# Kernel optimization log

Hardware: AMD Instinct MI355X
Metric: run time of the kernel (lower is better)

Reference implementation:

```python
import jax, jax.numpy as jnp
import numpy as np

N_BATCH, CH, HW, KERNEL, STRIDE, VC = 8, 256, 96, 8, 3, 512


def setup_inputs() -> dict:
    key = jax.random.key(0)
    k0, k1, k2, k3 = jax.random.split(key, 4)
    kk = KERNEL * KERNEL
    x = jax.random.normal(k0, (N_BATCH, CH, HW, HW), dtype=jnp.float32)
    # 1x1 conv weight [vc, ch, 1, 1] stored as [vc, ch]
    conv_w = jax.random.normal(k1, (VC, CH), dtype=jnp.float32) * 0.05
    # integrate_mask_activation: Linear(ch+kk, 3ch) -> LeakyReLU(0.2) -> Linear(3ch, ch) -> Tanh
    W1 = jax.random.normal(k2, (3 * CH, CH + kk), dtype=jnp.float32) * 0.02
    b1 = jnp.zeros((3 * CH,), dtype=jnp.float32)
    W2 = jax.random.normal(k3, (CH, 3 * CH), dtype=jnp.float32) * 0.02
    b2 = jnp.zeros((CH,), dtype=jnp.float32)
    return {"x": x, "conv_w": conv_w, "W1": W1, "b1": b1, "W2": W2, "b2": b2}


def _unfold(x, k, s):
    # torch.nn.Unfold(kernel=(k,k), stride=s) -> patches [n, L, c, k, k]
    n, c, h, w = x.shape
    oh = (h - k) // s + 1
    ow = (w - k) // s + 1
    ih = (jnp.arange(oh) * s)[:, None] + jnp.arange(k)[None, :]  # [oh, k]
    iw = (jnp.arange(ow) * s)[:, None] + jnp.arange(k)[None, :]  # [ow, k]
    p = x[:, :, ih, :]          # [n, c, oh, k, w]
    p = p[:, :, :, :, iw]       # [n, c, oh, k, ow, k]
    p = p.transpose(0, 2, 4, 1, 3, 5)  # [n, oh, ow, c, k, k]
    return p.reshape(n, oh * ow, c, k, k), oh * ow


def reference(x, conv_w, W1, b1, W2, b2):
    k = KERNEL
    kk = k * k
    n, c, h, w = x.shape
    patches, L = _unfold(x, k, STRIDE)           # [n, L, c, k, k]
    N = n * L
    p = patches.reshape(N, c, k, k)

    # GenerateMask_2_0: normalized similarity via 1x1 conv
    x_norm = jnp.sqrt((p ** 2).sum(1))           # [N, k, k]
    w_norm = jnp.sqrt((conv_w ** 2).sum(1))      # [vc]
    y = jnp.einsum('nchw,vc->nvhw', p, conv_w)   # [N, vc, k, k]
    y = y / (x_norm[:, None, :, :] * w_norm[None, :, None, None])

    vc = conv_w.shape[0]
    y_flat = y.reshape(N, vc * kk)
    idx = jnp.argmax(y_flat, axis=1)                       # topk(k=1)
    max_sim = jnp.take_along_axis(y_flat, idx[:, None], axis=1)  # [N, 1]
    max_ch = idx // kk                                     # codebook index [N]
    col = idx % kk                                         # spatial index [N]

    rows = jnp.arange(N)
    sim_map_max = y.reshape(N, vc, kk)[rows, max_ch]       # [N, kk]
    max_act = p.reshape(N, c, kk)[rows, :, col]            # [N, c]
    vc_vec = conv_w[max_ch]                                # [N, c]
    integ = max_act * max_sim + vc_vec * (1.0 - max_sim)   # blend with codebook

    # integrate_mask_activation MLP
    inp = jnp.concatenate([integ, sim_map_max], axis=1)    # [N, c + kk]
    h1 = inp @ W1.T + b1
    h1 = jnp.where(h1 > 0, h1, 0.2 * h1)                   # LeakyReLU(0.2)
    out = jnp.tanh(h1 @ W2.T + b2)                         # [N, c]
    return out.reshape(n, L, c)
```

## Files before the change

### kernel.cpp

```cpp
#include <hip/hip_runtime.h>
#include <hip/hip_fp16.h>
#include <math.h>

#define NB 8
#define CHN 256
#define HWD 96
#define PIXN (HWD*HWD)
#define TOTPIX (NB*PIXN)
#define VCN 512
#define OHW 30
#define LPP (OHW*OHW)
#define NPATCH (NB*LPP)
#define INPD 320
#define HID 768
#define MTP 456

typedef unsigned short u16;
typedef __attribute__((ext_vector_type(8))) short bf16x8;
typedef __attribute__((ext_vector_type(8))) unsigned short us8;
typedef __attribute__((ext_vector_type(4))) float f32x4;

__device__ __forceinline__ float f4c(const float4 v, int i){
  return i==0 ? v.x : i==1 ? v.y : i==2 ? v.z : v.w;
}
__device__ __forceinline__ u16 bfrn(float f){
  unsigned u = __float_as_uint(f);
  return (u16)((u + 0x7fffu + ((u>>16)&1u)) >> 16);
}
__device__ __forceinline__ float bf2f(u16 h){
  return __uint_as_float(((unsigned)h)<<16);
}


template<int NS>
__global__ __launch_bounds__(64) void wsplit_k(const float* __restrict__ src,
                                               u16* __restrict__ dst, int K){
  const int rt = blockIdx.x, kk = blockIdx.y, kkc = gridDim.y;
  const int lane = threadIdx.x, qr = lane>>4, col = lane&15;
  const float* s = src + (size_t)(rt*16+col)*K + kk*32 + qr*8;
  us8 h1, h2, h3;
  #pragma unroll
  for (int j=0;j<8;j++){
    float a = s[j];
    u16 x1 = bfrn(a);  float r1 = a - bf2f(x1);
    u16 x2 = bfrn(r1); float r2 = r1 - bf2f(x2);
    h1[j]=x1; h2[j]=x2; h3[j]=bfrn(r2);
  }
  size_t base = ((size_t)(rt*kkc + kk)*NS)*512 + lane*8;
  *(us8*)&dst[base]     = h1;
  *(us8*)&dst[base+512] = h2;
  if (NS == 3) *(us8*)&dst[base+1024] = h3;
}

__global__ void wnorm_k(const float* __restrict__ cw, float* __restrict__ invw){
  int v = blockIdx.x*256 + threadIdx.x;
  if (v >= VCN) return;
  const float* r = cw + (size_t)v*CHN;
  float s = 0.f;
  #pragma unroll 4
  for (int c=0;c<CHN;c++){ float t=r[c]; s = fmaf(t,t,s); }
  invw[v] = 1.0f/sqrtf(s);
}

__global__ void pixfin_k(const float* __restrict__ sumsq, float* __restrict__ invpix){
  int p = blockIdx.x*256 + threadIdx.x;
  if (p < TOTPIX) invpix[p] = rsqrtf(sumsq[p]);
}

__global__ __launch_bounds__(256) void xsplit_k(const float* __restrict__ x,
                                                u16* __restrict__ xf,
                                                float* __restrict__ sumsq){
  __shared__ float ts[64][65];
  __shared__ float ssq[64];
  const int p0 = blockIdx.x*64, c0 = blockIdx.y*64, img = blockIdx.z;
  const int t = threadIdx.x, lp = t&63, sub = t>>6;
  if (t < 64) ssq[t] = 0.f;
  const float* xb = x + (size_t)img*CHN*PIXN;
  #pragma unroll
  for (int r=0;r<16;r++){
    int cl = r*4 + sub;
    ts[cl][lp] = xb[(size_t)(c0+cl)*PIXN + p0 + lp];
  }
  __syncthreads();
  {
    float s = 0.f;
    #pragma unroll
    for (int r=0;r<16;r++){ float v = ts[r*4+sub][lp]; s = fmaf(v,v,s); }
    atomicAdd(&ssq[lp], s);
  }
  const int w = t>>6, lane = t&63;
  const int qr = lane>>4, pcol = lane&15;
  const size_t ptg = (size_t)(img*PIXN + p0)/16 + w;
  #pragma unroll
  for (int kkl=0;kkl<2;kkl++){
    const int kkg = (c0>>5) + kkl;
    us8 h1,h2,h3;
    #pragma unroll
    for (int j=0;j<8;j++){
      float a = ts[kkl*32 + qr*8 + j][w*16 + pcol];
      u16 x1 = bfrn(a);  float r1 = a - bf2f(x1);
      u16 x2 = bfrn(r1); float r2 = r1 - bf2f(x2);
      h1[j]=x1; h2[j]=x2; h3[j]=bfrn(r2);
    }
    size_t base = ((ptg*8 + kkg)*3)*512 + lane*8;
    *(us8*)&xf[base]      = h1;
    *(us8*)&xf[base+512]  = h2;
    *(us8*)&xf[base+1024] = h3;
  }
  __syncthreads();
  if (t < 64) atomicAdd(&sumsq[(size_t)img*PIXN + p0 + t], ssq[t]);
}

__global__ __launch_bounds__(256,4) void gemm_z_k(
    const u16* __restrict__ xf, const u16* __restrict__ wf,
    const float* __restrict__ invpix, const float* __restrict__ invw,
    float* __restrict__ mcand, int* __restrict__ vcand,
    __half* __restrict__ zf){
  __shared__ float rv[128][2];
  __shared__ int   ri[128][2];
  const int t = threadIdx.x;
  const int v0 = blockIdx.x*128, m0 = blockIdx.y*128;
  const int lane = t&63, wv = t>>6;
  const int mq = wv&1, nq = wv>>1;
  const int col = lane&15, qr = lane>>4;
  const size_t loff = (size_t)lane*8;
  const int ptA0 = (m0>>4) + mq*4;
  const int vtB0 = (v0>>4) + nq*4;
  f32x4 acc[4][4];
  #pragma unroll
  for (int i=0;i<4;i++)
    #pragma unroll
    for (int j=0;j<4;j++) acc[i][j] = (f32x4){0.f,0.f,0.f,0.f};

  for (int kk=0; kk<8; kk++){
    bf16x8 a[4][3];
    #pragma unroll
    for (int mi=0;mi<4;mi++){
      const size_t ab = (((size_t)(ptA0+mi)*8 + kk)*3)*512 + loff;
      a[mi][0] = *(const bf16x8*)&xf[ab];
      a[mi][1] = *(const bf16x8*)&xf[ab+512];
      a[mi][2] = *(const bf16x8*)&xf[ab+1024];
    }
    #pragma unroll
    for (int ni=0;ni<4;ni++){
      const size_t bb = (((size_t)(vtB0+ni)*8 + kk)*3)*512 + loff;
      const bf16x8 b1 = *(const bf16x8*)&wf[bb];
      const bf16x8 b2 = *(const bf16x8*)&wf[bb+512];
      const bf16x8 b3 = *(const bf16x8*)&wf[bb+1024];
      #pragma unroll
      for (int mi=0;mi<4;mi++){
        f32x4 c = acc[mi][ni];
        c = __builtin_amdgcn_mfma_f32_16x16x32_bf16(a[mi][0], b1, c, 0,0,0);
        c = __builtin_amdgcn_mfma_f32_16x16x32_bf16(a[mi][0], b2, c, 0,0,0);
        c = __builtin_amdgcn_mfma_f32_16x16x32_bf16(a[mi][1], b1, c, 0,0,0);
        c = __builtin_amdgcn_mfma_f32_16x16x32_bf16(a[mi][0], b3, c, 0,0,0);
        c = __builtin_amdgcn_mfma_f32_16x16x32_bf16(a[mi][1], b2, c, 0,0,0);
        c = __builtin_amdgcn_mfma_f32_16x16x32_bf16(a[mi][2], b1, c, 0,0,0);
        acc[mi][ni] = c;
      }
    }
  }
  float iw[4];
  #pragma unroll
  for (int ni=0; ni<4; ni++) iw[ni] = invw[v0 + nq*64 + ni*16 + col];
  #pragma unroll
  for (int mi=0; mi<4; mi++){
    #pragma unroll
    for (int r=0; r<4; r++){
      const int P = mq*64 + mi*16 + qr*4 + r;
      const float ip = invpix[m0 + P];
      float bz = -1e30f; int bvi = 0;
      #pragma unroll
      for (int ni=0; ni<4; ni++){
        const float z = f4c(*(const float4*)&acc[mi][ni], r) * ip * iw[ni];
        const int vv = v0 + nq*64 + ni*16 + col;
        zf[(size_t)(m0+P)*VCN + vv] = __float2half(z);
        if (z > bz){ bz = z; bvi = vv; }
      }
      #pragma unroll
      for (int off=1; off<16; off<<=1){
        const float oz = __shfl_xor(bz, off);
        const int  oi = __shfl_xor(bvi, off);
        if (oz > bz || (oz == bz && oi < bvi)){ bz = oz; bvi = oi; }
      }
      if (col == 0){ rv[P][nq] = bz; ri[P][nq] = bvi; }
    }
  }
  __syncthreads();
  if (t < 128){
    float z0 = rv[t][0], z1 = rv[t][1];
    int   i0 = ri[t][0], i1 = ri[t][1];
    float best = z0; int bi = i0;
    if (z1 > best || (z1 == best && i1 < bi)){ best = z1; bi = i1; }
    mcand[(size_t)(m0+t)*4 + blockIdx.x] = best;
    vcand[(size_t)(m0+t)*4 + blockIdx.x] = bi;
  }
}

__global__ __launch_bounds__(64) void select_k(
    const u16* __restrict__ xf, const float* __restrict__ cw,
    const __half* __restrict__ zf,
    const float* __restrict__ mcand, const int* __restrict__ vcand,
    u16* __restrict__ inpf){
  __shared__ float wlds[256];
  __shared__ float simv[64];
  const int q = blockIdx.x;
  const int lane = threadIdx.x;
  const int n = q / LPP, l = q % LPP;
  const int oy = l / OHW, ox = l % OHW;
  const int pl = (oy*3 + (lane >> 3))*HWD + (ox*3 + (lane & 7));
  const int p = n*PIXN + pl;
  const int rt = q >> 4, ql = q & 15;
  float best = -1e30f; int bv = 0;
  #pragma unroll
  for (int s=0;s<4;s++){
    float v2 = mcand[(size_t)p*4 + s];
    int i2 = vcand[(size_t)p*4 + s];
    if (v2 > best || (v2 == best && i2 < bv)){ best = v2; bv = i2; }
  }
  float val = best;
  int flat = bv*64 + lane;
  #pragma unroll
  for (int off=32; off>0; off>>=1){
    float ov = __shfl_xor(val, off);
    int of = __shfl_xor(flat, off);
    if (ov > val || (ov == val && of < flat)){ val = ov; flat = of; }
  }
  const int mch = flat >> 6;
  const int pos = flat & 63;
  const float ms = val;
  *(float4*)&wlds[lane*4] = *(const float4*)&cw[(size_t)mch*CHN + lane*4];
  simv[lane] = __half2float(zf[(size_t)p*VCN + mch]);
  __syncthreads();
  if (lane < 32){
    const int kk = lane >> 2, qr = lane & 3;
    const int wp = n*PIXN + (oy*3 + (pos>>3))*HWD + (ox*3 + (pos&7));
    const int wpt = wp >> 4, wpc = wp & 15;
    const size_t bb = (((size_t)wpt*8 + kk)*3)*512 + (qr*16 + wpc)*8;
    const us8 x1 = *(const us8*)&xf[bb];
    const us8 x2 = *(const us8*)&xf[bb+512];
    const us8 x3 = *(const us8*)&xf[bb+1024];
    const float om = 1.0f - ms;
    const int c0 = kk*32 + qr*8;
    us8 p1, p2;
    #pragma unroll
    for (int j=0;j<8;j++){
      float tv = bf2f(x1[j])+bf2f(x2[j])+bf2f(x3[j]);
      float v = fmaf(tv, ms, wlds[c0+j]*om);
      u16 s1 = bfrn(v);
      p1[j] = s1; p2[j] = bfrn(v - bf2f(s1));
    }
    const size_t ob = ((size_t)(rt*10 + kk)*2)*512 + (qr*16 + ql)*8;
    *(us8*)&inpf[ob]     = p1;
    *(us8*)&inpf[ob+512] = p2;
  }
  if (lane < 16){
    const int s = lane >> 3, kk = 8 + ((lane >> 2) & 1), qr = lane & 3;
    us8 pv;
    #pragma unroll
    for (int j=0;j<8;j++){
      float v = simv[(kk-8)*32 + qr*8 + j];
      u16 s1 = bfrn(v);
      pv[j] = (s == 0) ? s1 : bfrn(v - bf2f(s1));
    }
    const size_t ob = ((size_t)(rt*10 + kk)*2 + s)*512 + (qr*16 + ql)*8;
    *(us8*)&inpf[ob] = pv;
  }
}

__global__ __launch_bounds__(256,2) void mlp1_k(
    const u16* __restrict__ af, const u16* __restrict__ bf,
    const float* __restrict__ bias, u16* __restrict__ h1f){
  const int kkc = INPD >> 5;
  const int t = threadIdx.x;
  const int n0 = blockIdx.x*128, m0 = blockIdx.y*128;
  const int lane = t&63, wv = t>>6;
  const int mq = wv&1, nq = wv>>1;
  const int col = lane&15, qr = lane>>4;
  const size_t loff = (size_t)lane*8;
  const int ptA0 = (m0>>4) + mq*4;
  const int ntB0 = (n0>>4) + nq*4;
  f32x4 acc[4][4];
  #pragma unroll
  for (int i=0;i<4;i++)
    #pragma unroll
    for (int j=0;j<4;j++) acc[i][j] = (f32x4){0.f,0.f,0.f,0.f};

  for (int kk=0; kk<kkc; kk++){
    bf16x8 a[4][2];
    #pragma unroll
    for (int mi=0;mi<4;mi++){
      const size_t ab = (((size_t)(ptA0+mi)*kkc + kk)*2)*512 + loff;
      a[mi][0] = *(const bf16x8*)&af[ab];
      a[mi][1] = *(const bf16x8*)&af[ab+512];
    }
    #pragma unroll
    for (int ni=0;ni<4;ni++){
      const size_t bb = (((size_t)(ntB0+ni)*kkc + kk)*2)*512 + loff;
      const bf16x8 b1 = *(const bf16x8*)&bf[bb];
      const bf16x8 b2 = *(const bf16x8*)&bf[bb+512];
      #pragma unroll
      for (int mi=0;mi<4;mi++){
        f32x4 c = acc[mi][ni];
        c = __builtin_amdgcn_mfma_f32_16x16x32_bf16(a[mi][0], b1, c, 0,0,0);
        c = __builtin_amdgcn_mfma_f32_16x16x32_bf16(a[mi][0], b2, c, 0,0,0);
        c = __builtin_amdgcn_mfma_f32_16x16x32_bf16(a[mi][1], b1, c, 0,0,0);
        acc[mi][ni] = c;
      }
    }
  }
  float bb4[4];
  #pragma unroll
  for (int ni=0;ni<4;ni++) bb4[ni] = bias[n0 + nq*64 + ni*16 + col];
  #pragma unroll
  for (int mi=0;mi<4;mi++){
    const int rt2 = (m0>>4) + mq*4 + mi;
    #pragma unroll
    for (int r=0;r<4;r++){
      #pragma unroll
      for (int ni=0;ni<4;ni++){
        float v = f4c(*(const float4*)&acc[mi][ni], r) + bb4[ni];
        v = v > 0.f ? v : 0.2f*v;
        u16 s1 = bfrn(v);
        u16 s2 = bfrn(v - bf2f(s1));
        const int kk2 = (n0>>5) + nq*2 + (ni>>1);
        const int qn = (ni&1)*2 + (col>>3);
        const size_t ob = ((size_t)(rt2*24 + kk2)*2)*512 + (qn*16 + qr*4 + r)*8 + (col&7);
        h1f[ob] = s1; h1f[ob+512] = s2;
      }
    }
  }
}

__global__ __launch_bounds__(256,2) void mlp2_k(
    const u16* __restrict__ af, const u16* __restrict__ bf,
    const float* __restrict__ bias, float* __restrict__ C){
  const int kkc = HID >> 5;
  const int t = threadIdx.x;
  const int n0 = blockIdx.x*128, m0 = blockIdx.y*128;
  const int lane = t&63, wv = t>>6;
  const int mq = wv&1, nq = wv>>1;
  const int col = lane&15, qr = lane>>4;
  const size_t loff = (size_t)lane*8;
  const int ptA0 = (m0>>4) + mq*4;
  const int ntB0 = (n0>>4) + nq*4;
  f32x4 acc[4][4];
  #pragma unroll
  for (int i=0;i<4;i++)
    #pragma unroll
    for (int j=0;j<4;j++) acc[i][j] = (f32x4){0.f,0.f,0.f,0.f};

  for (int kk=0; kk<kkc; kk++){
    bf16x8 a[4][2];
    #pragma unroll
    for (int mi=0;mi<4;mi++){
      const size_t ab = (((size_t)(ptA0+mi)*kkc + kk)*2)*512 + loff;
      a[mi][0] = *(const bf16x8*)&af[ab];
      a[mi][1] = *(const bf16x8*)&af[ab+512];
    }
    #pragma unroll
    for (int ni=0;ni<4;ni++){
      const size_t bb = (((size_t)(ntB0+ni)*kkc + kk)*2)*512 + loff;
      const bf16x8 b1 = *(const bf16x8*)&bf[bb];
      const bf16x8 b2 = *(const bf16x8*)&bf[bb+512];
      #pragma unroll
      for (int mi=0;mi<4;mi++){
        f32x4 c = acc[mi][ni];
        c = __builtin_amdgcn_mfma_f32_16x16x32_bf16(a[mi][0], b1, c, 0,0,0);
        c = __builtin_amdgcn_mfma_f32_16x16x32_bf16(a[mi][0], b2, c, 0,0,0);
        c = __builtin_amdgcn_mfma_f32_16x16x32_bf16(a[mi][1], b1, c, 0,0,0);
        acc[mi][ni] = c;
      }
    }
  }
  float bb4[4];
  #pragma unroll
  for (int ni=0;ni<4;ni++) bb4[ni] = bias[n0 + nq*64 + ni*16 + col];
  #pragma unroll
  for (int mi=0;mi<4;mi++){
    #pragma unroll
    for (int r=0;r<4;r++){
      const int row = m0 + mq*64 + mi*16 + qr*4 + r;
      if (row < NPATCH){
        #pragma unroll
        for (int ni=0;ni<4;ni++){
          float v = f4c(*(const float4*)&acc[mi][ni], r) + bb4[ni];
          C[(size_t)row*CHN + n0 + nq*64 + ni*16 + col] = tanhf(v);
        }
      }
    }
  }
}

extern "C" void kernel_launch(void* const* d_in, const int* in_sizes, int n_in,
                              void* d_out, int out_size, void* d_ws, size_t ws_size,
                              hipStream_t stream){
  const float* x  = (const float*)d_in[0];
  const float* cw = (const float*)d_in[1];
  const float* W1 = (const float*)d_in[2];
  const float* b1 = (const float*)d_in[3];
  const float* W2 = (const float*)d_in[4];
  const float* b2 = (const float*)d_in[5];
  float* out = (float*)d_out;
  float* ws = (float*)d_ws;
  float* invpix = ws;
  float* invw   = invpix + TOTPIX;
  float* mcand  = invw + VCN;
  float* sumsq  = mcand;
  int*   vcand  = (int*)(mcand + (size_t)TOTPIX*4);
  u16*   xf     = (u16*)(vcand + (size_t)TOTPIX*4);
  u16*   wf     = xf + (size_t)(TOTPIX/16)*8*3*512;
  u16*   w1f    = wf + (size_t)32*8*3*512;
  u16*   w2f    = w1f + (size_t)48*10*2*512;
  u16*   inpf   = w2f + (size_t)16*24*2*512;
  __half* zf    = (__half*)(inpf + (size_t)MTP*10*2*512);
  u16*   h1f    = (u16*)zf;

  hipMemsetAsync(sumsq, 0, (size_t)TOTPIX*sizeof(float), stream);
  wsplit_k<3><<<dim3(VCN/16, CHN/32),64,0,stream>>>(cw, wf, CHN);
  wsplit_k<2><<<dim3(HID/16, INPD/32),64,0,stream>>>(W1, w1f, INPD);
  wsplit_k<2><<<dim3(CHN/16, HID/32),64,0,stream>>>(W2, w2f, HID);
  wnorm_k<<<2,256,0,stream>>>(cw, invw);
  xsplit_k<<<dim3(PIXN/64, CHN/64, NB),256,0,stream>>>(x, xf, sumsq);
  pixfin_k<<<TOTPIX/256,256,0,stream>>>(sumsq, invpix);
  gemm_z_k<<<dim3(VCN/128, TOTPIX/128),256,0,stream>>>(xf, wf, invpix, invw, mcand, vcand, zf);
  select_k<<<NPATCH,64,0,stream>>>(xf, cw, zf, mcand, vcand, inpf);
  mlp1_k<<<dim3(HID/128, (NPATCH+127)/128),256,0,stream>>>(inpf, w1f, b1, h1f);
  mlp2_k<<<dim3(CHN/128, (NPATCH+127)/128),256,0,stream>>>(h1f, w2f, b2, out);
}
```

Measured before the change: 368.4 us.

## Fuse input bf16 split and pixel norm into similarity GEMM via LDS staging

Drops the separate xsplit, pixfin and memset passes. Each GEMM block now reads 32 pixels of raw fp32 x, splits them into three bf16 parts in shared memory, and computes the pixel norms itself. Each block covers all 512 codebook vectors, so the argmax finishes inside the block and the 4-way candidate arrays go away. select_k now reads the raw x column directly. This removes the large xf intermediate's write and read traffic, at the cost of a smaller M tile per block, B fragments re-read from global by every block, and strided column reads of x.

After: 342.0 us. -7.2%, faster.

```diff
diff --git a/kernel.cpp b/kernel.cpp
--- a/kernel.cpp
+++ b/kernel.cpp
@@ -62,93 +62,74 @@
   invw[v] = 1.0f/sqrtf(s);
 }
 
-__global__ void pixfin_k(const float* __restrict__ sumsq, float* __restrict__ invpix){
-  int p = blockIdx.x*256 + threadIdx.x;
-  if (p < TOTPIX) invpix[p] = rsqrtf(sumsq[p]);
-}
-
-__global__ __launch_bounds__(256) void xsplit_k(const float* __restrict__ x,
-                                                u16* __restrict__ xf,
-                                                float* __restrict__ sumsq){
-  __shared__ float ts[64][65];
-  __shared__ float ssq[64];
-  const int p0 = blockIdx.x*64, c0 = blockIdx.y*64, img = blockIdx.z;
-  const int t = threadIdx.x, lp = t&63, sub = t>>6;
-  if (t < 64) ssq[t] = 0.f;
-  const float* xb = x + (size_t)img*CHN*PIXN;
-  #pragma unroll
-  for (int r=0;r<16;r++){
-    int cl = r*4 + sub;
-    ts[cl][lp] = xb[(size_t)(c0+cl)*PIXN + p0 + lp];
+__global__ __launch_bounds__(256,3) void gemm_z_k(
+    const float* __restrict__ x, const u16* __restrict__ wf,
+    const float* __restrict__ invw,
+    float* __restrict__ pbest, int* __restrict__ pbidx,
+    __half* __restrict__ zf){
+  __shared__ u16 afr[2*8*3*512];
+  __shared__ float ssq2[4][32];
+  __shared__ float rv[32][4];
+  __shared__ int   ri[32][4];
+  const int t = threadIdx.x;
+  const int wv = t>>6, lane = t&63;
+  const int col = lane&15, qr = lane>>4;
+  const size_t p0 = (size_t)blockIdx.x * 32;
+  const int img = (int)(p0 / PIXN);
+  const int pl0 = (int)(p0 % PIXN);
+
+  {
+    const int pi = t & 31, g2 = t >> 5;
+    const int mt = pi >> 4, fr = pi & 15;
+    const float* xb = x + ((size_t)img*CHN)*PIXN + pl0 + pi;
+    float s = 0.f;
+    unsigned* l32 = (unsigned*)afr;
+    #pragma unroll
+    for (int it=0; it<16; ++it){
+      const int c = it*16 + g2*2;
+      const float a0 = xb[(size_t)c*PIXN];
+      const float a1 = xb[(size_t)c*PIXN + PIXN];
+      s = fmaf(a0,a0,s); s = fmaf(a1,a1,s);
+      u16 x10 = bfrn(a0); float r10 = a0 - bf2f(x10);
+      u16 x20 = bfrn(r10);
+      u16 x30 = bfrn(r10 - bf2f(x20));
+      u16 x11 = bfrn(a1); float r11 = a1 - bf2f(x11);
+      u16 x21 = bfrn(r11);
+      u16 x31 = bfrn(r11 - bf2f(x21));
+      const int kk = c >> 5, kc = c & 31;
+      const unsigned b16 = (unsigned)(((mt*8 + kk)*3)*512 + ((kc>>3)*16 + fr)*8 + (kc&7));
+      l32[b16>>1]        = (unsigned)x10 | ((unsigned)x11<<16);
+      l32[(b16+512)>>1]  = (unsigned)x20 | ((unsigned)x21<<16);
+      l32[(b16+1024)>>1] = (unsigned)x30 | ((unsigned)x31<<16);
+    }
+    s += __shfl_xor(s, 32);
+    if (lane < 32) ssq2[wv][lane] = s;
   }
   __syncthreads();
-  {
-    float s = 0.f;
-    #pragma unroll
-    for (int r=0;r<16;r++){ float v = ts[r*4+sub][lp]; s = fmaf(v,v,s); }
-    atomicAdd(&ssq[lp], s);
-  }
-  const int w = t>>6, lane = t&63;
-  const int qr = lane>>4, pcol = lane&15;
-  const size_t ptg = (size_t)(img*PIXN + p0)/16 + w;
-  #pragma unroll
-  for (int kkl=0;kkl<2;kkl++){
-    const int kkg = (c0>>5) + kkl;
-    us8 h1,h2,h3;
-    #pragma unroll
-    for (int j=0;j<8;j++){
-      float a = ts[kkl*32 + qr*8 + j][w*16 + pcol];
-      u16 x1 = bfrn(a);  float r1 = a - bf2f(x1);
-      u16 x2 = bfrn(r1); float r2 = r1 - bf2f(x2);
-      h1[j]=x1; h2[j]=x2; h3[j]=bfrn(r2);
-    }
-    size_t base = ((ptg*8 + kkg)*3)*512 + lane*8;
-    *(us8*)&xf[base]      = h1;
-    *(us8*)&xf[base+512]  = h2;
-    *(us8*)&xf[base+1024] = h3;
-  }
-  __syncthreads();
-  if (t < 64) atomicAdd(&sumsq[(size_t)img*PIXN + p0 + t], ssq[t]);
-}
-
-__global__ __launch_bounds__(256,4) void gemm_z_k(
-    const u16* __restrict__ xf, const u16* __restrict__ wf,
-    const float* __restrict__ invpix, const float* __restrict__ invw,
-    float* __restrict__ mcand, int* __restrict__ vcand,
-    __half* __restrict__ zf){
-  __shared__ float rv[128][2];
-  __shared__ int   ri[128][2];
-  const int t = threadIdx.x;
-  const int v0 = blockIdx.x*128, m0 = blockIdx.y*128;
-  const int lane = t&63, wv = t>>6;
-  const int mq = wv&1, nq = wv>>1;
-  const int col = lane&15, qr = lane>>4;
+
+  f32x4 acc[2][8];
+  #pragma unroll
+  for (int i=0;i<2;i++)
+    #pragma unroll
+    for (int j=0;j<8;j++) acc[i][j] = (f32x4){0.f,0.f,0.f,0.f};
   const size_t loff = (size_t)lane*8;
-  const int ptA0 = (m0>>4) + mq*4;
-  const int vtB0 = (v0>>4) + nq*4;
-  f32x4 acc[4][4];
-  #pragma unroll
-  for (int i=0;i<4;i++)
-    #pragma unroll
-    for (int j=0;j<4;j++) acc[i][j] = (f32x4){0.f,0.f,0.f,0.f};
-
-  for (int kk=0; kk<8; kk++){
-    bf16x8 a[4][3];
-    #pragma unroll
-    for (int mi=0;mi<4;mi++){
-      const size_t ab = (((size_t)(ptA0+mi)*8 + kk)*3)*512 + loff;
-      a[mi][0] = *(const bf16x8*)&xf[ab];
-      a[mi][1] = *(const bf16x8*)&xf[ab+512];
-      a[mi][2] = *(const bf16x8*)&xf[ab+1024];
-    }
-    #pragma unroll
-    for (int ni=0;ni<4;ni++){
-      const size_t bb = (((size_t)(vtB0+ni)*8 + kk)*3)*512 + loff;
+  for (int kk=0; kk<8; ++kk){
+    bf16x8 a[2][3];
+    #pragma unroll
+    for (int mi=0; mi<2; ++mi){
+      const int ab = ((mi*8 + kk)*3)*512 + lane*8;
+      a[mi][0] = *(const bf16x8*)&afr[ab];
+      a[mi][1] = *(const bf16x8*)&afr[ab+512];
+      a[mi][2] = *(const bf16x8*)&afr[ab+1024];
+    }
+    #pragma unroll
+    for (int ni=0; ni<8; ++ni){
+      const size_t bb = (((size_t)(wv*8+ni)*8 + kk)*3)*512 + loff;
       const bf16x8 b1 = *(const bf16x8*)&wf[bb];
       const bf16x8 b2 = *(const bf16x8*)&wf[bb+512];
       const bf16x8 b3 = *(const bf16x8*)&wf[bb+1024];
       #pragma unroll
-      for (int mi=0;mi<4;mi++){
+      for (int mi=0; mi<2; ++mi){
         f32x4 c = acc[mi][ni];
         c = __builtin_amdgcn_mfma_f32_16x16x32_bf16(a[mi][0], b1, c, 0,0,0);
         c = __builtin_amdgcn_mfma_f32_16x16x32_bf16(a[mi][0], b2, c, 0,0,0);
@@ -160,21 +141,23 @@
       }
     }
   }
-  float iw[4];
-  #pragma unroll
-  for (int ni=0; ni<4; ni++) iw[ni] = invw[v0 + nq*64 + ni*16 + col];
-  #pragma unroll
-  for (int mi=0; mi<4; mi++){
-    #pragma unroll
-    for (int r=0; r<4; r++){
-      const int P = mq*64 + mi*16 + qr*4 + r;
-      const float ip = invpix[m0 + P];
+
+  float iw[8];
+  #pragma unroll
+  for (int ni=0;ni<8;ni++) iw[ni] = invw[wv*128 + ni*16 + col];
+  #pragma unroll
+  for (int mi=0;mi<2;mi++){
+    #pragma unroll
+    for (int r=0;r<4;r++){
+      const int P = mi*16 + qr*4 + r;
+      const float sq = ssq2[0][P] + ssq2[1][P] + ssq2[2][P] + ssq2[3][P];
+      const float ip = rsqrtf(sq);
       float bz = -1e30f; int bvi = 0;
       #pragma unroll
-      for (int ni=0; ni<4; ni++){
+      for (int ni=0;ni<8;ni++){
         const float z = f4c(*(const float4*)&acc[mi][ni], r) * ip * iw[ni];
-        const int vv = v0 + nq*64 + ni*16 + col;
-        zf[(size_t)(m0+P)*VCN + vv] = __float2half(z);
+        const int vv = wv*128 + ni*16 + col;
+        zf[(p0+P)*VCN + vv] = __float2half(z);
         if (z > bz){ bz = z; bvi = vv; }
       }
       #pragma unroll
@@ -183,26 +166,28 @@
         const int  oi = __shfl_xor(bvi, off);
         if (oz > bz || (oz == bz && oi < bvi)){ bz = oz; bvi = oi; }
       }
-      if (col == 0){ rv[P][nq] = bz; ri[P][nq] = bvi; }
+      if (col == 0){ rv[P][wv] = bz; ri[P][wv] = bvi; }
     }
   }
   __syncthreads();
-  if (t < 128){
-    float z0 = rv[t][0], z1 = rv[t][1];
-    int   i0 = ri[t][0], i1 = ri[t][1];
-    float best = z0; int bi = i0;
-    if (z1 > best || (z1 == best && i1 < bi)){ best = z1; bi = i1; }
-    mcand[(size_t)(m0+t)*4 + blockIdx.x] = best;
-    vcand[(size_t)(m0+t)*4 + blockIdx.x] = bi;
+  if (t < 32){
+    float best = rv[t][0]; int bi = ri[t][0];
+    #pragma unroll
+    for (int s=1;s<4;s++){
+      float z2 = rv[t][s]; int i2 = ri[t][s];
+      if (z2 > best || (z2 == best && i2 < bi)){ best = z2; bi = i2; }
+    }
+    pbest[p0+t] = best; pbidx[p0+t] = bi;
   }
 }
 
 __global__ __launch_bounds__(64) void select_k(
-    const u16* __restrict__ xf, const float* __restrict__ cw,
+    const float* __restrict__ x, const float* __restrict__ cw,
     const __half* __restrict__ zf,
-    const float* __restrict__ mcand, const int* __restrict__ vcand,
+    const float* __restrict__ pbest, const int* __restrict__ pbidx,
     u16* __restrict__ inpf){
   __shared__ float wlds[256];
+  __shared__ float xcol[256];
   __shared__ float simv[64];
   const int q = blockIdx.x;
   const int lane = threadIdx.x;
@@ -211,15 +196,8 @@
   const int pl = (oy*3 + (lane >> 3))*HWD + (ox*3 + (lane & 7));
   const int p = n*PIXN + pl;
   const int rt = q >> 4, ql = q & 15;
-  float best = -1e30f; int bv = 0;
-  #pragma unroll
-  for (int s=0;s<4;s++){
-    float v2 = mcand[(size_t)p*4 + s];
-    int i2 = vcand[(size_t)p*4 + s];
-    if (v2 > best || (v2 == best && i2 < bv)){ best = v2; bv = i2; }
-  }
-  float val = best;
-  int flat = bv*64 + lane;
+  float val = pbest[p];
+  int flat = pbidx[p]*64 + lane;
   #pragma unroll
   for (int off=32; off>0; off>>=1){
     float ov = __shfl_xor(val, off);
@@ -231,22 +209,19 @@
   const float ms = val;
   *(float4*)&wlds[lane*4] = *(const float4*)&cw[(size_t)mch*CHN + lane*4];
   simv[lane] = __half2float(zf[(size_t)p*VCN + mch]);
+  const int wpl = (oy*3 + (pos>>3))*HWD + (ox*3 + (pos&7));
+  const float* xb = x + (size_t)n*CHN*PIXN + wpl;
+  #pragma unroll
+  for (int j=0;j<4;j++) xcol[lane*4+j] = xb[(size_t)(lane*4+j)*PIXN];
   __syncthreads();
   if (lane < 32){
     const int kk = lane >> 2, qr = lane & 3;
-    const int wp = n*PIXN + (oy*3 + (pos>>3))*HWD + (ox*3 + (pos&7));
-    const int wpt = wp >> 4, wpc = wp & 15;
-    const size_t bb = (((size_t)wpt*8 + kk)*3)*512 + (qr*16 + wpc)*8;
-    const us8 x1 = *(const us8*)&xf[bb];
-    const us8 x2 = *(const us8*)&xf[bb+512];
-    const us8 x3 = *(const us8*)&xf[bb+1024];
     const float om = 1.0f - ms;
     const int c0 = kk*32 + qr*8;
     us8 p1, p2;
     #pragma unroll
     for (int j=0;j<8;j++){
-      float tv = bf2f(x1[j])+bf2f(x2[j])+bf2f(x3[j]);
-      float v = fmaf(tv, ms, wlds[c0+j]*om);
+      float v = fmaf(xcol[c0+j], ms, wlds[c0+j]*om);
       u16 s1 = bfrn(v);
       p1[j] = s1; p2[j] = bfrn(v - bf2f(s1));
     }
@@ -403,28 +378,22 @@
   const float* b2 = (const float*)d_in[5];
   float* out = (float*)d_out;
   float* ws = (float*)d_ws;
-  float* invpix = ws;
-  float* invw   = invpix + TOTPIX;
-  float* mcand  = invw + VCN;
-  float* sumsq  = mcand;
-  int*   vcand  = (int*)(mcand + (size_t)TOTPIX*4);
-  u16*   xf     = (u16*)(vcand + (size_t)TOTPIX*4);
-  u16*   wf     = xf + (size_t)(TOTPIX/16)*8*3*512;
-  u16*   w1f    = wf + (size_t)32*8*3*512;
-  u16*   w2f    = w1f + (size_t)48*10*2*512;
-  u16*   inpf   = w2f + (size_t)16*24*2*512;
-  __half* zf    = (__half*)(inpf + (size_t)MTP*10*2*512);
-  u16*   h1f    = (u16*)zf;
-
-  hipMemsetAsync(sumsq, 0, (size_t)TOTPIX*sizeof(float), stream);
+  float* invw  = ws;
+  float* pbest = invw + VCN;
+  int*   pbidx = (int*)(pbest + TOTPIX);
+  u16*   wf    = (u16*)(pbidx + TOTPIX);
+  u16*   w1f   = wf + (size_t)32*8*3*512;
+  u16*   w2f   = w1f + (size_t)48*10*2*512;
+  u16*   inpf  = w2f + (size_t)16*24*2*512;
+  __half* zf   = (__half*)(inpf + (size_t)MTP*10*2*512);
+  u16*   h1f   = (u16*)zf;
+
   wsplit_k<3><<<dim3(VCN/16, CHN/32),64,0,stream>>>(cw, wf, CHN);
   wsplit_k<2><<<dim3(HID/16, INPD/32),64,0,stream>>>(W1, w1f, INPD);
   wsplit_k<2><<<dim3(CHN/16, HID/32),64,0,stream>>>(W2, w2f, HID);
   wnorm_k<<<2,256,0,stream>>>(cw, invw);
-  xsplit_k<<<dim3(PIXN/64, CHN/64, NB),256,0,stream>>>(x, xf, sumsq);
-  pixfin_k<<<TOTPIX/256,256,0,stream>>>(sumsq, invpix);
-  gemm_z_k<<<dim3(VCN/128, TOTPIX/128),256,0,stream>>>(xf, wf, invpix, invw, mcand, vcand, zf);
-  select_k<<<NPATCH,64,0,stream>>>(xf, cw, zf, mcand, vcand, inpf);
+  gemm_z_k<<<TOTPIX/32,256,0,stream>>>(x, wf, invw, pbest, pbidx, zf);
+  select_k<<<NPATCH,64,0,stream>>>(x, cw, zf, pbest, pbidx, inpf);
   mlp1_k<<<dim3(HID/128, (NPATCH+127)/128),256,0,stream>>>(inpf, w1f, b1, h1f);
   mlp2_k<<<dim3(CHN/128, (NPATCH+127)/128),256,0,stream>>>(h1f, w2f, b2, out);
 }
```
